# Performance work log

Hardware: AMD Instinct MI355X
Metric: run time of the kernel (lower is better)

Reference implementation:

```python
import jax, jax.numpy as jnp
import numpy as np

MARGIN = 0.0625  # init kwarg `margin`; barrier = relu


def setup_inputs() -> dict:
    key = jax.random.key(0)
    k1, k2, k3, k4 = jax.random.split(key, 4)
    B, N, M = 64, 64, 100000
    return {
        "outputs": jax.random.normal(k1, (B, N, 3), dtype=jnp.float32),
        "c2ws": jax.random.normal(k2, (B, 4, 4), dtype=jnp.float32),
        "scene_scales": jax.random.uniform(k3, (B,), dtype=jnp.float32),
        "means": jax.random.normal(k4, (M, 3), dtype=jnp.float32),
    }


def reference(outputs, c2ws, scene_scales, means):
    # aff = R * s (per-batch scaled rotation block), trans = translation column
    aff = c2ws[:, :3, :3] * scene_scales[:, None, None]      # [B,3,3]
    trans = c2ws[:, :3, 3]                                   # [B,3]
    # retrajs = baddbmm(trans, outputs, aff.mT) = outputs @ aff^T + trans
    retrajs = jnp.einsum("bnj,bij->bni", outputs, aff) + trans[:, None, :]
    q = retrajs.reshape(-1, 3)                               # [Q,3], Q = B*N
    # Brute-force nearest neighbor (replaces kd_tree.query); torch_kdtree
    # returns SQUARED euclidean distances, so we keep d^2.
    # d2[q,m] = |q|^2 + |m|^2 - 2 q.m  -> [Q,M] (the dominant memory-bound op)
    d2 = (
        jnp.sum(q * q, axis=-1, keepdims=True)
        + jnp.sum(means * means, axis=-1)[None, :]
        - 2.0 * (q @ means.T)
    )
    dists = jnp.maximum(jnp.min(d2, axis=1), 0.0)            # [Q]
    loss = jnp.mean(jax.nn.relu(-(dists - MARGIN)))
    return loss
```

## Files before the change

### kernel.cpp

```cpp
#include <hip/hip_runtime.h>
#include <hip/hip_bf16.h>

#define MARGIN 0.0625f

#define P 4096
#define M 100000
#define G 500
#define CHUNK 200
#define QS 2
#define R 8
#define GRP 8
#define NITG (CHUNK / GRP)

typedef float float2v __attribute__((ext_vector_type(2)));

#define WS_XS_OFF      0
#define WS_YS_OFF      400000
#define WS_ZS_OFF      800000
#define WS_MS_OFF      1200000
#define WS_PARTIAL_OFF 1600000

__global__ __launch_bounds__(256) void prep_kernel(
    const float* __restrict__ means,
    float* __restrict__ xs, float* __restrict__ ys,
    float* __restrict__ zs, float* __restrict__ ms,
    float* __restrict__ out)
{
    int idx = blockIdx.x * 256 + threadIdx.x;
    if (idx == 0) out[0] = 0.0f;
    if (idx < M) {
        float x = means[3 * idx + 0];
        float y = means[3 * idx + 1];
        float z = means[3 * idx + 2];
        xs[idx] = -2.0f * x;
        ys[idx] = -2.0f * y;
        zs[idx] = -2.0f * z;
        ms[idx] = fmaf(x, x, fmaf(y, y, z * z));
    }
}

__global__ __launch_bounds__(256, 4) void nn_kernel(
    const float* __restrict__ outputs,
    const float* __restrict__ c2ws,
    const float* __restrict__ scales,
    const float* __restrict__ xs, const float* __restrict__ ys,
    const float* __restrict__ zs, const float* __restrict__ ms,
    float* __restrict__ partial)
{
    const int t  = threadIdx.x;
    const int g  = blockIdx.x;
    const int qs = blockIdx.y;
    const int pbase = qs * (P / QS);
    const int mbase = g * CHUNK;

    float2v qxs[R], qys[R], qzs[R], mn[R];
    float qq[R];
#pragma unroll
    for (int i = 0; i < R; ++i) {
        int p = pbase + i * 256 + t;
        int b = p >> 6;
        float s  = scales[b];
        float o0 = outputs[3 * p + 0];
        float o1 = outputs[3 * p + 1];
        float o2 = outputs[3 * p + 2];
        const float* cw = c2ws + b * 16;
        float q0 = fmaf(s, fmaf(cw[0],  o0, fmaf(cw[1],  o1, cw[2]  * o2)), cw[3]);
        float q1 = fmaf(s, fmaf(cw[4],  o0, fmaf(cw[5],  o1, cw[6]  * o2)), cw[7]);
        float q2 = fmaf(s, fmaf(cw[8],  o0, fmaf(cw[9],  o1, cw[10] * o2)), cw[11]);
        qq[i] = fmaf(q0, q0, fmaf(q1, q1, q2 * q2));
        qxs[i] = (float2v){q0, q0};
        qys[i] = (float2v){q1, q1};
        qzs[i] = (float2v){q2, q2};
        mn[i]  = (float2v){1e30f, 1e30f};
    }

#define LD2(arr, off) (*(const float2v*)((arr) + mbase + (off)))

    float2v cx[4], cy[4], cz[4], cm[4];
#pragma unroll
    for (int s = 0; s < 4; ++s) {
        cx[s] = LD2(xs, 2 * s); cy[s] = LD2(ys, 2 * s);
        cz[s] = LD2(zs, 2 * s); cm[s] = LD2(ms, 2 * s);
    }

    for (int kg = 0; kg < NITG; ++kg) {
        float2v nx[4], ny[4], nz[4], nm[4];
        if (kg < NITG - 1) {
            int nb = (kg + 1) * GRP;
#pragma unroll
            for (int s = 0; s < 4; ++s) {
                nx[s] = LD2(xs, nb + 2 * s); ny[s] = LD2(ys, nb + 2 * s);
                nz[s] = LD2(zs, nb + 2 * s); nm[s] = LD2(ms, nb + 2 * s);
            }
        }
#pragma unroll
        for (int s = 0; s < 4; ++s) {
#pragma unroll
            for (int i = 0; i < R; ++i) {
                float2v d = __builtin_elementwise_fma(qzs[i], cz[s],
                            __builtin_elementwise_fma(qys[i], cy[s],
                            __builtin_elementwise_fma(qxs[i], cx[s], cm[s])));
                mn[i] = __builtin_elementwise_min(mn[i], d);
            }
        }
        if (kg < NITG - 1) {
#pragma unroll
            for (int s = 0; s < 4; ++s) {
                cx[s] = nx[s]; cy[s] = ny[s]; cz[s] = nz[s]; cm[s] = nm[s];
            }
        }
    }
#undef LD2

#pragma unroll
    for (int i = 0; i < R; ++i) {
        int p = pbase + i * 256 + t;
        float m = fminf(mn[i][0], mn[i][1]);
        partial[g * P + p] = fmaxf(qq[i] + m, 0.0f);
    }
}

__global__ __launch_bounds__(256) void reduce_kernel(
    const float* __restrict__ partial,
    float* __restrict__ out)
{
    const int t   = threadIdx.x;
    const int qi  = t & 15;
    const int seg = t >> 4;
    const int q   = blockIdx.x * 16 + qi;

    float m = 1e30f;
    const int gbeg = seg * 32;
    const int gend = (gbeg + 32 < G) ? gbeg + 32 : G;
    for (int g = gbeg; g < gend; ++g)
        m = fminf(m, partial[g * P + q]);

    __shared__ float sm[16][16];
    sm[seg][qi] = m;
    __syncthreads();

    float v = 0.0f;
    if (t < 16) {
        float mm = sm[0][t];
#pragma unroll
        for (int s = 1; s < 16; ++s)
            mm = fminf(mm, sm[s][t]);
        v = fmaxf(MARGIN - mm, 0.0f) * (1.0f / (float)P);
    }
    if (t < 64) {
#pragma unroll
        for (int off = 32; off > 0; off >>= 1)
            v += __shfl_down(v, off, 64);
        if (t == 0)
            atomicAdd(out, v);
    }
}

extern "C" void kernel_launch(void* const* d_in, const int* in_sizes, int n_in,
                              void* d_out, int out_size, void* d_ws, size_t ws_size,
                              hipStream_t stream) {
    const float* outputs = (const float*)d_in[0];
    const float* c2ws    = (const float*)d_in[1];
    const float* scales  = (const float*)d_in[2];
    const float* means   = (const float*)d_in[3];

    char* ws = (char*)d_ws;
    float* xs      = (float*)(ws + WS_XS_OFF);
    float* ys      = (float*)(ws + WS_YS_OFF);
    float* zs      = (float*)(ws + WS_ZS_OFF);
    float* ms      = (float*)(ws + WS_MS_OFF);
    float* partial = (float*)(ws + WS_PARTIAL_OFF);
    float* out     = (float*)d_out;

    prep_kernel<<<(M + 255) / 256, 256, 0, stream>>>(means, xs, ys, zs, ms, out);
    nn_kernel<<<dim3(G, QS), 256, 0, stream>>>(outputs, c2ws, scales,
                                               xs, ys, zs, ms, partial);
    reduce_kernel<<<256, 256, 0, stream>>>(partial, out);
}
```

Before: 106.4 us.

## Stage mean chunks in LDS and split final reduction into two kernels

The NN kernel now loads each block's 200-point chunk of means into shared memory once and reads candidates from LDS in a simple unrolled loop. This replaces the register double-buffered global loads. The reduction is split into two kernels: a wider first pass over 16x16 blocks that min-reduces partials into a second workspace, then a small kernel that applies the margin and sums. This adds a sync and an extra launch, and may add LDS read overhead, in exchange for better reduction parallelism and coalescing.

```diff
diff --git a/kernel.cpp b/kernel.cpp
--- a/kernel.cpp
+++ b/kernel.cpp
@@ -7,10 +7,10 @@
 #define M 100000
 #define G 500
 #define CHUNK 200
+#define NPAIR (CHUNK / 2)
 #define QS 2
 #define R 8
-#define GRP 8
-#define NITG (CHUNK / GRP)
+#define HSEG 16
 
 typedef float float2v __attribute__((ext_vector_type(2)));
 
@@ -19,6 +19,7 @@
 #define WS_ZS_OFF      800000
 #define WS_MS_OFF      1200000
 #define WS_PARTIAL_OFF 1600000
+#define WS_PART2_OFF   9792000
 
 __global__ __launch_bounds__(256) void prep_kernel(
     const float* __restrict__ means,
@@ -53,6 +54,15 @@
     const int pbase = qs * (P / QS);
     const int mbase = g * CHUNK;
 
+    __shared__ float2v lxs[NPAIR], lys[NPAIR], lzs[NPAIR], lms[NPAIR];
+
+    if (t < NPAIR) {
+        lxs[t] = *(const float2v*)(xs + mbase + 2 * t);
+        lys[t] = *(const float2v*)(ys + mbase + 2 * t);
+        lzs[t] = *(const float2v*)(zs + mbase + 2 * t);
+        lms[t] = *(const float2v*)(ms + mbase + 2 * t);
+    }
+
     float2v qxs[R], qys[R], qzs[R], mn[R];
     float qq[R];
 #pragma unroll
@@ -74,43 +84,22 @@
         mn[i]  = (float2v){1e30f, 1e30f};
     }
 
-#define LD2(arr, off) (*(const float2v*)((arr) + mbase + (off)))
+    __syncthreads();
 
-    float2v cx[4], cy[4], cz[4], cm[4];
+#pragma unroll 4
+    for (int j = 0; j < NPAIR; ++j) {
+        float2v cx = lxs[j];
+        float2v cy = lys[j];
+        float2v cz = lzs[j];
+        float2v cm = lms[j];
 #pragma unroll
-    for (int s = 0; s < 4; ++s) {
-        cx[s] = LD2(xs, 2 * s); cy[s] = LD2(ys, 2 * s);
-        cz[s] = LD2(zs, 2 * s); cm[s] = LD2(ms, 2 * s);
-    }
-
-    for (int kg = 0; kg < NITG; ++kg) {
-        float2v nx[4], ny[4], nz[4], nm[4];
-        if (kg < NITG - 1) {
-            int nb = (kg + 1) * GRP;
-#pragma unroll
-            for (int s = 0; s < 4; ++s) {
-                nx[s] = LD2(xs, nb + 2 * s); ny[s] = LD2(ys, nb + 2 * s);
-                nz[s] = LD2(zs, nb + 2 * s); nm[s] = LD2(ms, nb + 2 * s);
-            }
-        }
-#pragma unroll
-        for (int s = 0; s < 4; ++s) {
-#pragma unroll
-            for (int i = 0; i < R; ++i) {
-                float2v d = __builtin_elementwise_fma(qzs[i], cz[s],
-                            __builtin_elementwise_fma(qys[i], cy[s],
-                            __builtin_elementwise_fma(qxs[i], cx[s], cm[s])));
-                mn[i] = __builtin_elementwise_min(mn[i], d);
-            }
-        }
-        if (kg < NITG - 1) {
-#pragma unroll
-            for (int s = 0; s < 4; ++s) {
-                cx[s] = nx[s]; cy[s] = ny[s]; cz[s] = nz[s]; cm[s] = nm[s];
-            }
+        for (int i = 0; i < R; ++i) {
+            float2v d = __builtin_elementwise_fma(qzs[i], cz,
+                        __builtin_elementwise_fma(qys[i], cy,
+                        __builtin_elementwise_fma(qxs[i], cx, cm)));
+            mn[i] = __builtin_elementwise_min(mn[i], d);
         }
     }
-#undef LD2
 
 #pragma unroll
     for (int i = 0; i < R; ++i) {
@@ -120,40 +109,50 @@
     }
 }
 
-__global__ __launch_bounds__(256) void reduce_kernel(
+__global__ __launch_bounds__(256) void reduce1_kernel(
     const float* __restrict__ partial,
-    float* __restrict__ out)
+    float* __restrict__ partial2)
 {
-    const int t   = threadIdx.x;
-    const int qi  = t & 15;
-    const int seg = t >> 4;
-    const int q   = blockIdx.x * 16 + qi;
+    const int t = threadIdx.x;
+    const int s = blockIdx.x;
+    const int h = blockIdx.y;
+    const int q = s * 256 + t;
+
+    const int gbeg = h * 32;
+    const int gend = (gbeg + 32 < G) ? gbeg + 32 : G;
 
     float m = 1e30f;
-    const int gbeg = seg * 32;
-    const int gend = (gbeg + 32 < G) ? gbeg + 32 : G;
+#pragma unroll 4
     for (int g = gbeg; g < gend; ++g)
         m = fminf(m, partial[g * P + q]);
 
-    __shared__ float sm[16][16];
-    sm[seg][qi] = m;
+    partial2[h * P + q] = m;
+}
+
+__global__ __launch_bounds__(256) void reduce2_kernel(
+    const float* __restrict__ partial2,
+    float* __restrict__ out)
+{
+    const int t = threadIdx.x;
+    const int q = blockIdx.x * 256 + t;
+
+    float m = 1e30f;
+#pragma unroll
+    for (int h = 0; h < HSEG; ++h)
+        m = fminf(m, partial2[h * P + q]);
+
+    float v = fmaxf(MARGIN - m, 0.0f) * (1.0f / (float)P);
+
+#pragma unroll
+    for (int off = 32; off > 0; off >>= 1)
+        v += __shfl_down(v, off, 64);
+
+    __shared__ float lds[4];
+    int wid = t >> 6;
+    if ((t & 63) == 0) lds[wid] = v;
     __syncthreads();
-
-    float v = 0.0f;
-    if (t < 16) {
-        float mm = sm[0][t];
-#pragma unroll
-        for (int s = 1; s < 16; ++s)
-            mm = fminf(mm, sm[s][t]);
-        v = fmaxf(MARGIN - mm, 0.0f) * (1.0f / (float)P);
-    }
-    if (t < 64) {
-#pragma unroll
-        for (int off = 32; off > 0; off >>= 1)
-            v += __shfl_down(v, off, 64);
-        if (t == 0)
-            atomicAdd(out, v);
-    }
+    if (t == 0)
+        atomicAdd(out, lds[0] + lds[1] + lds[2] + lds[3]);
 }
 
 extern "C" void kernel_launch(void* const* d_in, const int* in_sizes, int n_in,
@@ -165,15 +164,17 @@
     const float* means   = (const float*)d_in[3];
 
     char* ws = (char*)d_ws;
-    float* xs      = (float*)(ws + WS_XS_OFF);
-    float* ys      = (float*)(ws + WS_YS_OFF);
-    float* zs      = (float*)(ws + WS_ZS_OFF);
-    float* ms      = (float*)(ws + WS_MS_OFF);
-    float* partial = (float*)(ws + WS_PARTIAL_OFF);
-    float* out     = (float*)d_out;
+    float* xs       = (float*)(ws + WS_XS_OFF);
+    float* ys       = (float*)(ws + WS_YS_OFF);
+    float* zs       = (float*)(ws + WS_ZS_OFF);
+    float* ms       = (float*)(ws + WS_MS_OFF);
+    float* partial  = (float*)(ws + WS_PARTIAL_OFF);
+    float* partial2 = (float*)(ws + WS_PART2_OFF);
+    float* out      = (float*)d_out;
 
     prep_kernel<<<(M + 255) / 256, 256, 0, stream>>>(means, xs, ys, zs, ms, out);
     nn_kernel<<<dim3(G, QS), 256, 0, stream>>>(outputs, c2ws, scales,
                                                xs, ys, zs, ms, partial);
-    reduce_kernel<<<256, 256, 0, stream>>>(partial, out);
+    reduce1_kernel<<<dim3(16, HSEG), 256, 0, stream>>>(partial, partial2);
+    reduce2_kernel<<<16, 256, 0, stream>>>(partial2, out);
 }
```

Measured after the change: 105.5 us. Within noise of the previous version (-0.8%).
